# Optimization experiments

Hardware: AMD Instinct MI355X
Metric: run time of the kernel (lower is better)

## Reference

```python
import jax, jax.numpy as jnp
import numpy as np
from math import sqrt


def setup_inputs() -> dict:
    key = jax.random.key(0)
    k1, k2, k3 = jax.random.split(key, 3)
    B, L, H, E = 2, 2048, 16, 64
    queries = jax.random.normal(k1, (B, L, H, E), dtype=jnp.float32)
    keys = jax.random.normal(k2, (B, L, H, E), dtype=jnp.float32)
    values = jax.random.normal(k3, (B, L, H, E), dtype=jnp.float32)
    return {"queries": queries, "keys": keys, "values": values}


def reference(queries, keys, values):
    # queries: [B,L,H,E], keys: [B,S,H,E], values: [B,S,H,D]
    B, L, H, E = queries.shape
    S = keys.shape[1]
    scale = 1.0 / sqrt(E)
    # raw scores [B,H,L,S]
    scores = jnp.einsum('blhe,bshe->bhls', queries, keys)
    # triangular causal mask (True above diagonal -> masked)
    causal = jnp.triu(jnp.ones((L, S), dtype=bool), k=1)  # [L,S]
    scores = jnp.where(causal[None, None, :, :], -jnp.inf, scores)
    A = jax.nn.softmax(scale * scores, axis=-1)  # dropout p=0 -> identity
    V = jnp.einsum('bhls,bshd->blhd', A, values)
    return V
```

## Files before the change

kernel.cpp:

```cpp
#include <hip/hip_runtime.h>

typedef __attribute__((ext_vector_type(2))) __fp16 fp16x2;
typedef __attribute__((ext_vector_type(4))) _Float16 half4;
typedef __attribute__((ext_vector_type(8))) _Float16 half8;
typedef __attribute__((ext_vector_type(4))) float floatx4;

typedef union { half8 h8; half4 h4[2]; } h8split;

#define B_SZ  2
#define L_SEQ 2048
#define NH    16
#define EDIM  64
#define LOG2E 1.4426950408889634f
#define QSCALE (0.125f * LOG2E)

__device__ __forceinline__ int swz(int s, int ch) {
    return ch ^ (((s & 7) + 2 * (s >> 4)) & 7);
}

__global__ __launch_bounds__(256, 1)
void convert_kv(const float* __restrict__ K, const float* __restrict__ V,
                _Float16* __restrict__ Kh, _Float16* __restrict__ Vt)
{
    __shared__ __align__(16) _Float16 Tile[64 * 64];
    const int st = blockIdx.x & 31;
    const int h  = (blockIdx.x >> 5) & 15;
    const int b  = blockIdx.x >> 9;
    const int s0 = st * 64;
    const int t  = threadIdx.x;
    const int r  = t >> 2, c = t & 3;
    const size_t bh   = (size_t)b * NH + h;
    const size_t src  = (((size_t)b * L_SEQ + s0 + r) * NH + h) * EDIM + c * 16;
    const size_t cbase = bh * (size_t)(L_SEQ * EDIM) + (size_t)st * 4096;

    {
        const float4* kp = (const float4*)(K + src);
        float4 f[4];
#pragma unroll
        for (int i = 0; i < 4; ++i) f[i] = kp[i];
        _Float16 tmp[16];
#pragma unroll
        for (int i = 0; i < 4; ++i) {
            fp16x2 a  = __builtin_amdgcn_cvt_pkrtz(f[i].x, f[i].y);
            fp16x2 b2 = __builtin_amdgcn_cvt_pkrtz(f[i].z, f[i].w);
            tmp[4*i+0] = (_Float16)a[0];  tmp[4*i+1] = (_Float16)a[1];
            tmp[4*i+2] = (_Float16)b2[0]; tmp[4*i+3] = (_Float16)b2[1];
        }
        _Float16* kd = Kh + cbase + (size_t)(r >> 4) * 1024 + (c >> 1) * 512 + (r & 15) * 8;
        *(half8*)(kd + (((2 * c)     & 3) * 128)) = *(half8*)&tmp[0];
        *(half8*)(kd + (((2 * c + 1) & 3) * 128)) = *(half8*)&tmp[8];
    }
    {
        const float4* vp = (const float4*)(V + src);
        float4 f[4];
#pragma unroll
        for (int i = 0; i < 4; ++i) f[i] = vp[i];
        _Float16 tmp[16];
#pragma unroll
        for (int i = 0; i < 4; ++i) {
            fp16x2 a  = __builtin_amdgcn_cvt_pkrtz(f[i].x, f[i].y);
            fp16x2 b2 = __builtin_amdgcn_cvt_pkrtz(f[i].z, f[i].w);
            tmp[4*i+0] = (_Float16)a[0];  tmp[4*i+1] = (_Float16)a[1];
            tmp[4*i+2] = (_Float16)b2[0]; tmp[4*i+3] = (_Float16)b2[1];
        }
        _Float16* base = &Tile[r * 64];
        *(half8*)(base + swz(r, 2 * c)     * 8) = *(half8*)&tmp[0];
        *(half8*)(base + swz(r, 2 * c + 1) * 8) = *(half8*)&tmp[8];
    }
    __syncthreads();
    {
        const int d = t >> 2, seg = t & 3;
        _Float16 tmp[16];
#pragma unroll
        for (int i = 0; i < 16; ++i) {
            const int s = seg * 16 + i;
            tmp[i] = Tile[s * 64 + swz(s, d >> 3) * 8 + (d & 7)];
        }
        _Float16* vd = Vt + cbase + (size_t)seg * 1024 + (d >> 5) * 512
                       + (d & 15) * 8 + ((d >> 4) & 1) * 4;
#pragma unroll
        for (int kg = 0; kg < 4; ++kg)
            *(half4*)(vd + kg * 128) = *(half4*)&tmp[kg * 4];
    }
}

__global__ __launch_bounds__(128, 2)
void fa_fwd(const float* __restrict__ Q, const _Float16* __restrict__ Kh,
            const _Float16* __restrict__ Vt, float* __restrict__ O)
{
    __shared__ __align__(16) _Float16 Kb[2][4096];
    __shared__ __align__(16) _Float16 Vb[2][4096];

    const int i  = blockIdx.x;
    const int bh = i & 31;
    const int v  = i >> 5;
    const int u  = v & 7, j = v >> 3;
    const int tile = (j == 0) ? (31 - u) : (j == 1) ? u : (j == 2) ? (23 - u) : (8 + u);
    const int b    = bh >> 4;
    const int h    = bh & 15;
    const int wid  = threadIdx.x >> 6;
    const int lane = threadIdx.x & 63;
    const int ln16 = lane & 15;
    const int quad = lane >> 4;
    const int qrow0 = tile * 64;
    const int nch   = tile + 1;
    const int t16   = threadIdx.x * 16;
    const int lane8 = lane * 8;

    half8 qfA[2], qfB[2];
#pragma unroll
    for (int g = 0; g < 2; ++g) {
        const float4* qp = (const float4*)(Q + (((size_t)b * L_SEQ + qrow0 + wid * 16 + g * 32 + ln16) * NH + h) * EDIM + quad * 8);
        float4 f0 = qp[0], f1 = qp[1];
        float4 f2 = qp[8], f3 = qp[9];
        fp16x2 t0 = __builtin_amdgcn_cvt_pkrtz(f0.x * QSCALE, f0.y * QSCALE);
        fp16x2 t1 = __builtin_amdgcn_cvt_pkrtz(f0.z * QSCALE, f0.w * QSCALE);
        fp16x2 t2 = __builtin_amdgcn_cvt_pkrtz(f1.x * QSCALE, f1.y * QSCALE);
        fp16x2 t3 = __builtin_amdgcn_cvt_pkrtz(f1.z * QSCALE, f1.w * QSCALE);
        qfA[g][0] = (_Float16)t0[0]; qfA[g][1] = (_Float16)t0[1];
        qfA[g][2] = (_Float16)t1[0]; qfA[g][3] = (_Float16)t1[1];
        qfA[g][4] = (_Float16)t2[0]; qfA[g][5] = (_Float16)t2[1];
        qfA[g][6] = (_Float16)t3[0]; qfA[g][7] = (_Float16)t3[1];
        t0 = __builtin_amdgcn_cvt_pkrtz(f2.x * QSCALE, f2.y * QSCALE);
        t1 = __builtin_amdgcn_cvt_pkrtz(f2.z * QSCALE, f2.w * QSCALE);
        t2 = __builtin_amdgcn_cvt_pkrtz(f3.x * QSCALE, f3.y * QSCALE);
        t3 = __builtin_amdgcn_cvt_pkrtz(f3.z * QSCALE, f3.w * QSCALE);
        qfB[g][0] = (_Float16)t0[0]; qfB[g][1] = (_Float16)t0[1];
        qfB[g][2] = (_Float16)t1[0]; qfB[g][3] = (_Float16)t1[1];
        qfB[g][4] = (_Float16)t2[0]; qfB[g][5] = (_Float16)t2[1];
        qfB[g][6] = (_Float16)t3[0]; qfB[g][7] = (_Float16)t3[1];
    }

    const char* kgb = (const char*)(Kh + (size_t)bh * (L_SEQ * EDIM));
    const char* vgb = (const char*)(Vt + (size_t)bh * (L_SEQ * EDIM));

#pragma unroll
    for (int k = 0; k < 4; ++k) {
        *(half8*)((char*)Kb[0] + t16 + k * 2048) = *(const half8*)(kgb + t16 + k * 2048);
        *(half8*)((char*)Vb[0] + t16 + k * 2048) = *(const half8*)(vgb + t16 + k * 2048);
    }
    __syncthreads();

    floatx4 acc[4][2];
#pragma unroll
    for (int dt = 0; dt < 4; ++dt)
#pragma unroll
        for (int g = 0; g < 2; ++g) acc[dt][g] = (floatx4){0.f, 0.f, 0.f, 0.f};
    float lp[2] = {0.f, 0.f};

    for (int it = 0; it < nch; ++it) {
        const bool last = (it + 1 >= nch);
        half8 stK[4], stV[4];
        if (!last) {
            const char* ks = kgb + (size_t)(it + 1) * 8192;
            const char* vs = vgb + (size_t)(it + 1) * 8192;
#pragma unroll
            for (int k = 0; k < 4; ++k) {
                stK[k] = *(const half8*)(ks + t16 + k * 2048);
                stV[k] = *(const half8*)(vs + t16 + k * 2048);
            }
        }

        const _Float16* kc = Kb[it & 1];
        const _Float16* vv = Vb[it & 1];
        const bool masked = (it == nch - 1);
#pragma unroll
        for (int s = 0; s < 4; ++s) {
            half8 k0 = *(const half8*)(kc + s * 1024 + lane8);
            half8 k1 = *(const half8*)(kc + s * 1024 + 512 + lane8);
            h8split u01, u23;
            u01.h8 = *(const half8*)(vv + s * 1024 + lane8);
            u23.h8 = *(const half8*)(vv + s * 1024 + 512 + lane8);

#pragma unroll
            for (int g = 0; g < 2; ++g) {
                floatx4 z = (floatx4){0.f, 0.f, 0.f, 0.f};
                z = __builtin_amdgcn_mfma_f32_16x16x32_f16(k0, qfA[g], z, 0, 0, 0);
                floatx4 st = __builtin_amdgcn_mfma_f32_16x16x32_f16(k1, qfB[g], z, 0, 0, 0);

                float p[4];
#pragma unroll
                for (int r = 0; r < 4; ++r) {
                    float e = __builtin_amdgcn_exp2f(st[r]);
                    if (masked) {
                        const int key = it * 64 + s * 16 + quad * 4 + r;
                        e = (key <= qrow0 + wid * 16 + g * 32 + ln16) ? e : 0.0f;
                    }
                    p[r] = e;
                }
                lp[g] += (p[0] + p[1]) + (p[2] + p[3]);
                fp16x2 lo = __builtin_amdgcn_cvt_pkrtz(p[0], p[1]);
                fp16x2 hi = __builtin_amdgcn_cvt_pkrtz(p[2], p[3]);
                half4 pf;
                pf[0] = (_Float16)lo[0]; pf[1] = (_Float16)lo[1];
                pf[2] = (_Float16)hi[0]; pf[3] = (_Float16)hi[1];

                acc[0][g] = __builtin_amdgcn_mfma_f32_16x16x16f16(u01.h4[0], pf, acc[0][g], 0, 0, 0);
                acc[1][g] = __builtin_amdgcn_mfma_f32_16x16x16f16(u01.h4[1], pf, acc[1][g], 0, 0, 0);
                acc[2][g] = __builtin_amdgcn_mfma_f32_16x16x16f16(u23.h4[0], pf, acc[2][g], 0, 0, 0);
                acc[3][g] = __builtin_amdgcn_mfma_f32_16x16x16f16(u23.h4[1], pf, acc[3][g], 0, 0, 0);
            }
        }

        if (!last) {
            char* kd = (char*)Kb[(it + 1) & 1];
            char* vd = (char*)Vb[(it + 1) & 1];
#pragma unroll
            for (int k = 0; k < 4; ++k) {
                *(half8*)(kd + t16 + k * 2048) = stK[k];
                *(half8*)(vd + t16 + k * 2048) = stV[k];
            }
            __syncthreads();
        }
    }

#pragma unroll
    for (int g = 0; g < 2; ++g) {
        float l = lp[g];
        l += __shfl_xor(l, 16);
        l += __shfl_xor(l, 32);
        const float inv = 1.0f / l;
        float* op = O + (((size_t)b * L_SEQ + qrow0 + wid * 16 + g * 32 + ln16) * NH + h) * EDIM;
#pragma unroll
        for (int dt = 0; dt < 4; ++dt) {
            float4 ov = {acc[dt][g][0] * inv, acc[dt][g][1] * inv,
                         acc[dt][g][2] * inv, acc[dt][g][3] * inv};
            *(float4*)(op + dt * 16 + quad * 4) = ov;
        }
    }
}

extern "C" void kernel_launch(void* const* d_in, const int* in_sizes, int n_in,
                              void* d_out, int out_size, void* d_ws, size_t ws_size,
                              hipStream_t stream) {
    const float* Q = (const float*)d_in[0];
    const float* K = (const float*)d_in[1];
    const float* V = (const float*)d_in[2];
    float* O = (float*)d_out;
    _Float16* Kh = (_Float16*)d_ws;
    _Float16* Vt = Kh + (size_t)B_SZ * NH * L_SEQ * EDIM;
    convert_kv<<<dim3(B_SZ * NH * (L_SEQ / 64)), dim3(256), 0, stream>>>(K, V, Kh, Vt);
    fa_fwd<<<dim3(32 * 32), dim3(128), 0, stream>>>(Q, Kh, Vt, O);
}
```

Measured before the change: 121.9 us.

## Double query tile to 128 rows with 256-thread blocks sharing K/V loads

Each attention block now covers 128 query rows with four waves instead of 64 rows with two waves, so every staged K/V chunk in shared memory is reused by twice as many queries. Global-to-LDS traffic per query is halved, and each thread loads half as many elements per chunk. The grid shrinks to 512 blocks with a simpler tile ordering. In exchange, parallelism drops and causal load balance gets coarser, and the last two chunks now need masking.

Measured after the change: 135.3 us. +11.0%, slower.

```diff
diff --git a/kernel.cpp b/kernel.cpp
--- a/kernel.cpp
+++ b/kernel.cpp
@@ -84,7 +84,7 @@
     }
 }
 
-__global__ __launch_bounds__(128, 2)
+__global__ __launch_bounds__(256, 2)
 void fa_fwd(const float* __restrict__ Q, const _Float16* __restrict__ Kh,
             const _Float16* __restrict__ Vt, float* __restrict__ O)
 {
@@ -94,23 +94,22 @@
     const int i  = blockIdx.x;
     const int bh = i & 31;
     const int v  = i >> 5;
-    const int u  = v & 7, j = v >> 3;
-    const int tile = (j == 0) ? (31 - u) : (j == 1) ? u : (j == 2) ? (23 - u) : (8 + u);
+    const int tile = (v < 8) ? (15 - v) : (v - 8);
     const int b    = bh >> 4;
     const int h    = bh & 15;
     const int wid  = threadIdx.x >> 6;
     const int lane = threadIdx.x & 63;
     const int ln16 = lane & 15;
     const int quad = lane >> 4;
-    const int qrow0 = tile * 64;
-    const int nch   = tile + 1;
+    const int qrow0 = tile * 128;
+    const int nch   = 2 * tile + 2;
     const int t16   = threadIdx.x * 16;
     const int lane8 = lane * 8;
 
     half8 qfA[2], qfB[2];
 #pragma unroll
     for (int g = 0; g < 2; ++g) {
-        const float4* qp = (const float4*)(Q + (((size_t)b * L_SEQ + qrow0 + wid * 16 + g * 32 + ln16) * NH + h) * EDIM + quad * 8);
+        const float4* qp = (const float4*)(Q + (((size_t)b * L_SEQ + qrow0 + wid * 16 + g * 64 + ln16) * NH + h) * EDIM + quad * 8);
         float4 f0 = qp[0], f1 = qp[1];
         float4 f2 = qp[8], f3 = qp[9];
         fp16x2 t0 = __builtin_amdgcn_cvt_pkrtz(f0.x * QSCALE, f0.y * QSCALE);
@@ -134,11 +133,10 @@
     const char* kgb = (const char*)(Kh + (size_t)bh * (L_SEQ * EDIM));
     const char* vgb = (const char*)(Vt + (size_t)bh * (L_SEQ * EDIM));
 
-#pragma unroll
-    for (int k = 0; k < 4; ++k) {
-        *(half8*)((char*)Kb[0] + t16 + k * 2048) = *(const half8*)(kgb + t16 + k * 2048);
-        *(half8*)((char*)Vb[0] + t16 + k * 2048) = *(const half8*)(vgb + t16 + k * 2048);
-    }
+    *(half8*)((char*)Kb[0] + t16)        = *(const half8*)(kgb + t16);
+    *(half8*)((char*)Kb[0] + 4096 + t16) = *(const half8*)(kgb + 4096 + t16);
+    *(half8*)((char*)Vb[0] + t16)        = *(const half8*)(vgb + t16);
+    *(half8*)((char*)Vb[0] + 4096 + t16) = *(const half8*)(vgb + 4096 + t16);
     __syncthreads();
 
     floatx4 acc[4][2];
@@ -150,20 +148,19 @@
 
     for (int it = 0; it < nch; ++it) {
         const bool last = (it + 1 >= nch);
-        half8 stK[4], stV[4];
+        half8 sk0, sk1, sv0, sv1;
         if (!last) {
             const char* ks = kgb + (size_t)(it + 1) * 8192;
             const char* vs = vgb + (size_t)(it + 1) * 8192;
-#pragma unroll
-            for (int k = 0; k < 4; ++k) {
-                stK[k] = *(const half8*)(ks + t16 + k * 2048);
-                stV[k] = *(const half8*)(vs + t16 + k * 2048);
-            }
+            sk0 = *(const half8*)(ks + t16);
+            sk1 = *(const half8*)(ks + 4096 + t16);
+            sv0 = *(const half8*)(vs + t16);
+            sv1 = *(const half8*)(vs + 4096 + t16);
         }
 
         const _Float16* kc = Kb[it & 1];
         const _Float16* vv = Vb[it & 1];
-        const bool masked = (it == nch - 1);
+        const bool masked = (it >= nch - 2);
 #pragma unroll
         for (int s = 0; s < 4; ++s) {
             half8 k0 = *(const half8*)(kc + s * 1024 + lane8);
@@ -184,7 +181,7 @@
                     float e = __builtin_amdgcn_exp2f(st[r]);
                     if (masked) {
                         const int key = it * 64 + s * 16 + quad * 4 + r;
-                        e = (key <= qrow0 + wid * 16 + g * 32 + ln16) ? e : 0.0f;
+                        e = (key <= qrow0 + wid * 16 + g * 64 + ln16) ? e : 0.0f;
                     }
                     p[r] = e;
                 }
@@ -205,11 +202,10 @@
         if (!last) {
             char* kd = (char*)Kb[(it + 1) & 1];
             char* vd = (char*)Vb[(it + 1) & 1];
-#pragma unroll
-            for (int k = 0; k < 4; ++k) {
-                *(half8*)(kd + t16 + k * 2048) = stK[k];
-                *(half8*)(vd + t16 + k * 2048) = stV[k];
-            }
+            *(half8*)(kd + t16)        = sk0;
+            *(half8*)(kd + 4096 + t16) = sk1;
+            *(half8*)(vd + t16)        = sv0;
+            *(half8*)(vd + 4096 + t16) = sv1;
             __syncthreads();
         }
     }
@@ -220,7 +216,7 @@
         l += __shfl_xor(l, 16);
         l += __shfl_xor(l, 32);
         const float inv = 1.0f / l;
-        float* op = O + (((size_t)b * L_SEQ + qrow0 + wid * 16 + g * 32 + ln16) * NH + h) * EDIM;
+        float* op = O + (((size_t)b * L_SEQ + qrow0 + wid * 16 + g * 64 + ln16) * NH + h) * EDIM;
 #pragma unroll
         for (int dt = 0; dt < 4; ++dt) {
             float4 ov = {acc[dt][g][0] * inv, acc[dt][g][1] * inv,
@@ -240,5 +236,5 @@
     _Float16* Kh = (_Float16*)d_ws;
     _Float16* Vt = Kh + (size_t)B_SZ * NH * L_SEQ * EDIM;
     convert_kv<<<dim3(B_SZ * NH * (L_SEQ / 64)), dim3(256), 0, stream>>>(K, V, Kh, Vt);
-    fa_fwd<<<dim3(32 * 32), dim3(128), 0, stream>>>(Q, Kh, Vt, O);
-}
+    fa_fwd<<<dim3(16 * 32), dim3(256), 0, stream>>>(Q, Kh, Vt, O);
+}
```
